# Performance work log

Measured on AMD Instinct MI355X. Metric: run time of the kernel, lower is better.

Reference implementation:

```python
import math
import jax, jax.numpy as jnp
import numpy as np

B, S, D, H = 4, 2048, 1024, 16
HD = D // H  # head_dim = 64


def setup_inputs() -> dict:
    key = jax.random.key(0)
    ks = jax.random.split(key, 10)
    scale = 1.0 / math.sqrt(D)
    inp = {
        "q": jax.random.normal(ks[0], (B, S, D), dtype=jnp.float32),
        "q_mask": jax.random.bernoulli(ks[1], 0.9, (B, S)),
        "Wq": jax.random.normal(ks[2], (D, D), dtype=jnp.float32) * scale,
        "bq": jax.random.normal(ks[3], (D,), dtype=jnp.float32) * 0.01,
        "Wk": jax.random.normal(ks[4], (D, D), dtype=jnp.float32) * scale,
        "bk": jax.random.normal(ks[5], (D,), dtype=jnp.float32) * 0.01,
        "Wv": jax.random.normal(ks[6], (D, D), dtype=jnp.float32) * scale,
        "bv": jax.random.normal(ks[7], (D,), dtype=jnp.float32) * 0.01,
        "Wo": jax.random.normal(ks[8], (D, D), dtype=jnp.float32) * scale,
        "bo": jax.random.normal(ks[9], (D,), dtype=jnp.float32) * 0.01,
    }
    return inp


def reference(q, q_mask, Wq, bq, Wk, bk, Wv, bv, Wo, bo):
    # Self-attention: k = v = q, kv_mask = q_mask (per forward() defaults).
    # Linear projections (nn.Linear: x @ W^T + b), then split heads -> (b, h, s, hd)
    def proj(x, W, b):
        y = jnp.einsum("bsd,ed->bse", x, W) + b
        return y.reshape(B, S, H, HD).transpose(0, 2, 1, 3)

    qh = proj(q, Wq, bq)
    kh = proj(q, Wk, bk)
    vh = proj(q, Wv, bv)

    # Scaled dot-product scores: (b, h, s_q, s_k), scaled by sqrt(head_dim)
    scores = jnp.einsum("bhqd,bhkd->bhqk", qh, kh) / math.sqrt(HD)

    # merge_masks: q_mask & kv_mask (kv_mask == q_mask), broadcast over heads
    merged = q_mask[:, :, None] & q_mask[:, None, :]          # (b, s_q, s_k)
    scores = jnp.where(merged[:, None, :, :], scores, -jnp.inf)

    # softmax over keys; fully-masked (padded query) rows -> nan -> 0
    attn = jax.nn.softmax(scores, axis=-1)
    attn = jnp.nan_to_num(attn, nan=0.0)
    # dropout prob = 0 (eval) -> no-op

    out = jnp.einsum("bhqk,bhkd->bhqd", attn, vh)             # (b, h, s, hd)
    out = out.transpose(0, 2, 1, 3).reshape(B, S, D)
    return jnp.einsum("bsd,ed->bse", out, Wo) + bo
```

## Files before the change

### kernel.cpp

```cpp
#include <hip/hip_runtime.h>
#include <hip/hip_bf16.h>
#include <stdint.h>

typedef __bf16 v8y __attribute__((ext_vector_type(8)));
typedef _Float16 v8h __attribute__((ext_vector_type(8)));
typedef float  v4f __attribute__((ext_vector_type(4)));
typedef float  v16f __attribute__((ext_vector_type(16)));
typedef __hip_bfloat16 bf;

#define AS1 __attribute__((address_space(1)))
#define AS3 __attribute__((address_space(3)))

__device__ __forceinline__ void gload16(const bf* g, bf* l) {
  __builtin_amdgcn_global_load_lds((const AS1 uint32_t*)g, (AS3 uint32_t*)l, 16, 0, 0);
}

static constexpr int Bb = 4, Sdim = 2048, Ddim = 1024, Hn = 16, HD = 64;
static constexpr int Kd = 1024, Nd = 1024;
static constexpr int WSZ = Ddim * Ddim;
static constexpr float NEG = -1e30f;

__device__ __forceinline__ void stc(bf* p, float v)    { *p = __float2bfloat16(v); }
__device__ __forceinline__ void stc(float* p, float v) { *p = v; }

__device__ __forceinline__ uint32_t pkbf(float lo, float hi_) {
  union { bf h[2]; uint32_t u; } t;
  t.h[0] = __float2bfloat16(lo);
  t.h[1] = __float2bfloat16(hi_);
  return t.u;
}

__global__ __launch_bounds__(256)
void cvt_f16(const float* __restrict__ src, uint16_t* __restrict__ dst, int n) {
  const int i = (blockIdx.x * 256 + threadIdx.x) * 8;
  if (i >= n) return;
  const float4 a = *reinterpret_cast<const float4*>(src + i);
  const float4 b = *reinterpret_cast<const float4*>(src + i + 4);
  const float x[8] = {a.x, a.y, a.z, a.w, b.x, b.y, b.z, b.w};
  union { uint16_t h[8]; uint4 u; } U;
#pragma unroll
  for (int j = 0; j < 8; ++j) U.h[j] = __builtin_bit_cast(uint16_t, (_Float16)x[j]);
  *reinterpret_cast<uint4*>(dst + i) = U.u;
}

__global__ __launch_bounds__(256)
void cvt_w(const float* __restrict__ Wq, const float* __restrict__ Wk,
           const float* __restrict__ Wv, const float* __restrict__ Wo,
           uint16_t* __restrict__ wb) {
  const int i = (blockIdx.x * 256 + threadIdx.x) * 8;
  const int z = blockIdx.y;
  const float* src = z == 0 ? Wq : (z == 1 ? Wk : (z == 2 ? Wv : Wo));
  uint16_t* dst = wb + (size_t)WSZ * z;
  const float4 a = *reinterpret_cast<const float4*>(src + i);
  const float4 b = *reinterpret_cast<const float4*>(src + i + 4);
  const float x[8] = {a.x, a.y, a.z, a.w, b.x, b.y, b.z, b.w};
  union { uint16_t h[8]; uint4 u; } U;
  if (z < 3) {
#pragma unroll
    for (int j = 0; j < 8; ++j) U.h[j] = __builtin_bit_cast(uint16_t, (_Float16)x[j]);
  } else {
#pragma unroll
    for (int j = 0; j < 8; ++j) U.h[j] = __builtin_bit_cast(uint16_t, __float2bfloat16(x[j]));
  }
  *reinterpret_cast<uint4*>(dst + i) = U.u;
}

__global__ __launch_bounds__(256)
void maskpack(const int* __restrict__ mask, uint64_t* __restrict__ mp) {
  const int gid = blockIdx.x * 256 + threadIdx.x;
  const uint64_t bal = __ballot(mask[gid] != 0);
  if ((threadIdx.x & 63) == 0) mp[gid >> 6] = bal;
}

template<bool F16, bool HEADLAYOUT, typename TC>
__global__ __launch_bounds__(256)
void gemm_bt(const bf* __restrict__ A,
             const bf* __restrict__ W0, const bf* __restrict__ W1, const bf* __restrict__ W2,
             const float* __restrict__ b0, const float* __restrict__ b1, const float* __restrict__ b2,
             TC* __restrict__ C0, TC* __restrict__ C1, TC* __restrict__ C2)
{
  const int z = blockIdx.z;
  const bf* Wh = z == 0 ? W0 : (z == 1 ? W1 : W2);
  const float* bias = z == 0 ? b0 : (z == 1 ? b1 : b2);
  TC* C = z == 0 ? C0 : (z == 1 ? C1 : C2);

  constexpr int PL = 128 * 32;
  __shared__ __align__(16) bf As[PL];
  __shared__ __align__(16) bf Bs[PL];

  const int tid = threadIdx.x;
  const int w = tid >> 6, l = tid & 63;
  const int m0 = blockIdx.x * 128, n0 = blockIdx.y * 128;
  const int wm = (w & 1) * 64, wn = (w >> 1) * 64;
  const int lr = l & 15, quad = l >> 4;
  const int srow = l >> 2, sk = (l & 3) * 8;

  v4f acc[4][4] = {};

  for (int kt = 0; kt < Kd; kt += 32) {
    __syncthreads();
#pragma unroll
    for (int c = 0; c < 2; ++c) {
      const int rb = (c * 4 + w) * 16;
      const int64_t goff = (int64_t)(rb + srow) * Kd + kt + sk;
      gload16(A + (int64_t)m0 * Kd + goff, As + rb * 32);
      gload16(Wh + (int64_t)n0 * Kd + goff, Bs + rb * 32);
    }
    __syncthreads();

    v8y afh[4], bfh[4];
#pragma unroll
    for (int i = 0; i < 4; ++i) {
      const int ro = (wm + i * 16 + lr) * 32 + quad * 8;
      const int co = (wn + i * 16 + lr) * 32 + quad * 8;
      afh[i] = *reinterpret_cast<const v8y*>(As + ro);
      bfh[i] = *reinterpret_cast<const v8y*>(Bs + co);
    }
#pragma unroll
    for (int i = 0; i < 4; ++i)
#pragma unroll
      for (int j = 0; j < 4; ++j) {
        if constexpr (F16) {
          acc[i][j] = __builtin_amdgcn_mfma_f32_16x16x32_f16(
              __builtin_bit_cast(v8h, afh[i]), __builtin_bit_cast(v8h, bfh[j]),
              acc[i][j], 0, 0, 0);
        } else {
          acc[i][j] = __builtin_amdgcn_mfma_f32_16x16x32_bf16(afh[i], bfh[j], acc[i][j], 0, 0, 0);
        }
      }
  }

#pragma unroll
  for (int j = 0; j < 4; ++j) {
    const int gn = n0 + wn + j * 16 + lr;
    const float bv = bias[gn];
#pragma unroll
    for (int i = 0; i < 4; ++i) {
#pragma unroll
      for (int r = 0; r < 4; ++r) {
        const int gm = m0 + wm + i * 16 + quad * 4 + r;
        float v = acc[i][j][r] + bv;
        if (HEADLAYOUT) {
          const int bidx = gm >> 11, s = gm & (Sdim - 1);
          const int h = gn >> 6, hd = gn & (HD - 1);
          if (z == 0) v *= 0.125f;
          const int64_t idx = (z == 2)
            ? ((int64_t)(bidx * Hn + h) * HD + hd) * Sdim + s
            : (((int64_t)(bidx * Hn + h) * Sdim + s) << 6) + hd;
          stc(&C[idx], v);
        } else {
          stc(&C[(int64_t)gm * Nd + gn], v);
        }
      }
    }
  }
}

__global__ __launch_bounds__(256)
void attn_kernel(const bf* __restrict__ qh, const bf* __restrict__ kh,
                 const bf* __restrict__ vt, const int* __restrict__ mask,
                 const uint64_t* __restrict__ mp, bf* __restrict__ outp)
{
  __shared__ __align__(16) bf sm[2][8192];

  const int tid = threadIdx.x;
  const int w = tid >> 6, l = tid & 63;
  const int lq = l & 31, hi = l >> 5;
  const int bh = blockIdx.x, b = bh >> 4;
  const int q0 = blockIdx.y * 128 + w * 32;
  const int64_t base = (int64_t)bh * (Sdim * HD);

  v8y qf[4];
#pragma unroll
  for (int s = 0; s < 4; ++s)
    qf[s] = *reinterpret_cast<const v8y*>(qh + base + (int64_t)(q0 + lq) * 64 + s * 16 + hi * 8);

  const bool qmask = mask[b * Sdim + q0 + lq] != 0;

  float m_i = NEG, l_i = 0.f;
  v16f oacc[2] = {};

  const int srcperm = ((l & 7) ^ (l >> 3)) * 8;
  const int srow8 = l >> 3;

#define STAGE(bufi, ktn)                                                          \
  {                                                                               \
    bf* KB_ = sm[bufi];                                                           \
    bf* VB_ = sm[bufi] + 4096;                                                    \
    _Pragma("unroll")                                                             \
    for (int i_ = 0; i_ < 2; ++i_) {                                              \
      const int c_ = w * 2 + i_;                                                  \
      const int row_ = c_ * 8 + srow8;                                            \
      gload16(kh + base + (int64_t)((ktn) + row_) * 64 + srcperm, KB_ + c_ * 512);\
      gload16(vt + base + (int64_t)row_ * Sdim + (ktn) + srcperm, VB_ + c_ * 512);\
    }                                                                             \
  }

  STAGE(0, 0);
  asm volatile("s_waitcnt vmcnt(0)" ::: "memory");
  __syncthreads();

  for (int kt = 0; kt < Sdim; kt += 64) {
    const int buf = (kt >> 6) & 1;
    if (kt + 64 < Sdim) STAGE(buf ^ 1, kt + 64);

    const bf* KB = sm[buf];
    const bf* VB = sm[buf] + 4096;

    v16f sacc[2] = {};
    __builtin_amdgcn_s_setprio(1);
#pragma unroll
    for (int n = 0; n < 2; ++n) {
      const int row = n * 32 + lq;
      const int swz = (row & 7);
#pragma unroll
      for (int s = 0; s < 4; ++s) {
        const int colE = ((2 * s + hi) ^ swz) * 8;
        v8y kf = *reinterpret_cast<const v8y*>(KB + row * 64 + colE);
        sacc[n] = __builtin_amdgcn_mfma_f32_32x32x16_bf16(kf, qf[s], sacc[n], 0, 0, 0);
      }
    }
    __builtin_amdgcn_s_setprio(0);

    const uint64_t km64 = mp[b * 32 + (kt >> 6)];
    const uint32_t km0 = (uint32_t)km64 >> (4 * hi);
    const uint32_t km1 = (uint32_t)(km64 >> 32) >> (4 * hi);
#pragma unroll
    for (int r = 0; r < 16; ++r) {
      const uint32_t bit = 1u << ((r & 3) + 8 * (r >> 2));
      sacc[0][r] = (km0 & bit) ? sacc[0][r] : NEG;
      sacc[1][r] = (km1 & bit) ? sacc[1][r] : NEG;
    }

    float mx = NEG;
#pragma unroll
    for (int n = 0; n < 2; ++n)
#pragma unroll
      for (int r = 0; r < 16; ++r) mx = fmaxf(mx, sacc[n][r]);
    mx = fmaxf(mx, __shfl_xor(mx, 32));
    const float mn = fmaxf(m_i, mx);
    const float alpha = __expf(m_i - mn);
    m_i = mn;

    float sum = 0.f;
#pragma unroll
    for (int n = 0; n < 2; ++n)
#pragma unroll
      for (int r = 0; r < 16; ++r) {
        const float p = __expf(sacc[n][r] - mn);
        sacc[n][r] = p;
        sum += p;
      }
    sum += __shfl_xor(sum, 32);
    l_i = l_i * alpha + sum;
#pragma unroll
    for (int d2 = 0; d2 < 2; ++d2)
#pragma unroll
      for (int r = 0; r < 16; ++r) oacc[d2][r] *= alpha;

    uint32_t pq[8][2];
#pragma unroll
    for (int n = 0; n < 2; ++n)
#pragma unroll
      for (int g = 0; g < 4; ++g) {
        pq[n * 4 + g][0] = pkbf(sacc[n][g * 4 + 0], sacc[n][g * 4 + 1]);
        pq[n * 4 + g][1] = pkbf(sacc[n][g * 4 + 2], sacc[n][g * 4 + 3]);
      }

#pragma unroll
    for (int ks = 0; ks < 4; ++ks) {
      const uint32_t own0 = hi ? pq[2 * ks + 1][0] : pq[2 * ks][0];
      const uint32_t own1 = hi ? pq[2 * ks + 1][1] : pq[2 * ks][1];
      const uint32_t snd0 = hi ? pq[2 * ks][0] : pq[2 * ks + 1][0];
      const uint32_t snd1 = hi ? pq[2 * ks][1] : pq[2 * ks + 1][1];
      const uint32_t rc0 = (uint32_t)__shfl_xor((int)snd0, 32);
      const uint32_t rc1 = (uint32_t)__shfl_xor((int)snd1, 32);
      union { uint32_t u[4]; v8y v; } pf;
      pf.u[0] = hi ? rc0 : own0;
      pf.u[1] = hi ? rc1 : own1;
      pf.u[2] = hi ? own0 : rc0;
      pf.u[3] = hi ? own1 : rc1;
      __builtin_amdgcn_s_setprio(1);
#pragma unroll
      for (int d2 = 0; d2 < 2; ++d2) {
        const int row = d2 * 32 + lq;
        const int colE = ((2 * ks + hi) ^ (row & 7)) * 8;
        v8y vf = *reinterpret_cast<const v8y*>(VB + row * 64 + colE);
        oacc[d2] = __builtin_amdgcn_mfma_f32_32x32x16_bf16(vf, pf.v, oacc[d2], 0, 0, 0);
      }
      __builtin_amdgcn_s_setprio(0);
    }

    asm volatile("s_waitcnt vmcnt(0)" ::: "memory");
    __syncthreads();
  }
#undef STAGE

  const float inv = qmask ? 1.f / l_i : 0.f;
  bf* orow = outp + ((int64_t)b * Sdim + q0 + lq) * Ddim + (bh & 15) * 64;
#pragma unroll
  for (int d2 = 0; d2 < 2; ++d2)
#pragma unroll
    for (int g = 0; g < 4; ++g) {
      union { bf h[4]; uint2 u; } pk;
#pragma unroll
      for (int c = 0; c < 4; ++c) pk.h[c] = __float2bfloat16(oacc[d2][g * 4 + c] * inv);
      *reinterpret_cast<uint2*>(orow + d2 * 32 + 8 * g + 4 * hi) = pk.u;
    }
}

extern "C" void kernel_launch(void* const* d_in, const int* in_sizes, int n_in,
                              void* d_out, int out_size, void* d_ws, size_t ws_size,
                              hipStream_t stream) {
  (void)in_sizes; (void)n_in; (void)out_size; (void)ws_size;
  const float* q    = (const float*)d_in[0];
  const int*   mask = (const int*)d_in[1];
  const float* Wq = (const float*)d_in[2];
  const float* bq = (const float*)d_in[3];
  const float* Wk = (const float*)d_in[4];
  const float* bk = (const float*)d_in[5];
  const float* Wv = (const float*)d_in[6];
  const float* bv = (const float*)d_in[7];
  const float* Wo = (const float*)d_in[8];
  const float* bo = (const float*)d_in[9];
  float* out = (float*)d_out;
  bf* ws  = (bf*)d_ws;

  constexpr int SZ = Bb * Sdim * Ddim;

  bf* qc  = ws;
  bf* qhp = ws + (size_t)SZ;
  bf* khp = ws + 2 * (size_t)SZ;
  bf* vtp = ws + 3 * (size_t)SZ;
  bf* wb  = ws + 4 * (size_t)SZ;
  bf* wq = wb;
  bf* wk = wb + WSZ;
  bf* wv = wb + 2 * (size_t)WSZ;
  bf* wo = wb + 3 * (size_t)WSZ;
  uint64_t* mpk = (uint64_t*)(wb + 4 * (size_t)WSZ);
  bf* ao = qc;

  cvt_f16<<<dim3(SZ / 2048), dim3(256), 0, stream>>>(q, (uint16_t*)qc, SZ);
  cvt_w<<<dim3(WSZ / 2048, 4), dim3(256), 0, stream>>>(Wq, Wk, Wv, Wo, (uint16_t*)wb);
  maskpack<<<dim3(32), dim3(256), 0, stream>>>(mask, mpk);

  gemm_bt<true, true, bf><<<dim3(64, 8, 3), dim3(256), 0, stream>>>(
      qc, wq, wk, wv, bq, bk, bv, qhp, khp, vtp);

  attn_kernel<<<dim3(Bb * Hn, Sdim / 128), dim3(256), 0, stream>>>(qhp, khp, vtp, mask, mpk, ao);

  gemm_bt<false, false, float><<<dim3(64, 8, 1), dim3(256), 0, stream>>>(
      ao, wo, wo, wo, bo, bo, bo, out, out, out);
}
```

Baseline: 354.8 us.

## Rework attention softmax: exp2 scaling, lazy rescale, MFMA row sums, bitmask-AND masking

Folds log2(e) into the Q scale so the softmax can use exp2 directly. Skips the rescale of the running max and accumulator unless the new max exceeds the old one by more than a threshold. Replaces the per-lane sum reduction with an extra MFMA against a ones vector, and applies the key mask by ANDing the packed bf16 probabilities with precomputed 32-bit mask words. This removes per-element select, sum and scaling ALU work from the inner loop. In exchange it adds one MFMA per k-step, and the lazy rescale lets unnormalised probabilities grow to about 2^11, which reduces bf16 headroom.

```diff
diff --git a/kernel.cpp b/kernel.cpp
--- a/kernel.cpp
+++ b/kernel.cpp
@@ -19,6 +19,7 @@
 static constexpr int Kd = 1024, Nd = 1024;
 static constexpr int WSZ = Ddim * Ddim;
 static constexpr float NEG = -1e30f;
+static constexpr float QSCALE = 0.18033688011112042f;
 
 __device__ __forceinline__ void stc(bf* p, float v)    { *p = __float2bfloat16(v); }
 __device__ __forceinline__ void stc(float* p, float v) { *p = v; }
@@ -66,10 +67,19 @@
 }
 
 __global__ __launch_bounds__(256)
-void maskpack(const int* __restrict__ mask, uint64_t* __restrict__ mp) {
+void maskpack(const int* __restrict__ mask, uint32_t* __restrict__ mw) {
   const int gid = blockIdx.x * 256 + threadIdx.x;
   const uint64_t bal = __ballot(mask[gid] != 0);
-  if ((threadIdx.x & 63) == 0) mp[gid >> 6] = bal;
+  const int l = threadIdx.x & 63;
+  if (l < 32) {
+    const int bt = gid >> 6;
+    const int h = l >> 4, n = (l >> 3) & 1, g = (l >> 1) & 3, wi = l & 1;
+    const int k0 = n * 32 + g * 8 + h * 4 + wi * 2;
+    uint32_t wv = 0;
+    if ((bal >> k0) & 1) wv |= 0x0000FFFFu;
+    if ((bal >> (k0 + 1)) & 1) wv |= 0xFFFF0000u;
+    mw[bt * 32 + l] = wv;
+  }
 }
 
 template<bool F16, bool HEADLAYOUT, typename TC>
@@ -143,7 +153,7 @@
         if (HEADLAYOUT) {
           const int bidx = gm >> 11, s = gm & (Sdim - 1);
           const int h = gn >> 6, hd = gn & (HD - 1);
-          if (z == 0) v *= 0.125f;
+          if (z == 0) v *= QSCALE;
           const int64_t idx = (z == 2)
             ? ((int64_t)(bidx * Hn + h) * HD + hd) * Sdim + s
             : (((int64_t)(bidx * Hn + h) * Sdim + s) << 6) + hd;
@@ -159,7 +169,7 @@
 __global__ __launch_bounds__(256)
 void attn_kernel(const bf* __restrict__ qh, const bf* __restrict__ kh,
                  const bf* __restrict__ vt, const int* __restrict__ mask,
-                 const uint64_t* __restrict__ mp, bf* __restrict__ outp)
+                 const uint32_t* __restrict__ mw, bf* __restrict__ outp)
 {
   __shared__ __align__(16) bf sm[2][8192];
 
@@ -177,8 +187,13 @@
 
   const bool qmask = mask[b * Sdim + q0 + lq] != 0;
 
-  float m_i = NEG, l_i = 0.f;
+  union { uint32_t u[4]; v8y v; } ONES;
+#pragma unroll
+  for (int j = 0; j < 4; ++j) ONES.u[j] = 0x3F803F80u;
+
+  float m_i = NEG;
   v16f oacc[2] = {};
+  v16f sumacc = {};
 
   const int srcperm = ((l & 7) ^ (l >> 3)) * 8;
   const int srow8 = l >> 3;
@@ -204,6 +219,14 @@
     const int buf = (kt >> 6) & 1;
     if (kt + 64 < Sdim) STAGE(buf ^ 1, kt + 64);
 
+    union { uint32_t u[16]; uint4 q[4]; } MW;
+    {
+      const uint4* mwp = reinterpret_cast<const uint4*>(
+          mw + ((size_t)(b * 32 + (kt >> 6)) * 32) + hi * 16);
+#pragma unroll
+      for (int j = 0; j < 4; ++j) MW.q[j] = mwp[j];
+    }
+
     const bf* KB = sm[buf];
     const bf* VB = sm[buf] + 4096;
 
@@ -222,49 +245,36 @@
     }
     __builtin_amdgcn_s_setprio(0);
 
-    const uint64_t km64 = mp[b * 32 + (kt >> 6)];
-    const uint32_t km0 = (uint32_t)km64 >> (4 * hi);
-    const uint32_t km1 = (uint32_t)(km64 >> 32) >> (4 * hi);
-#pragma unroll
-    for (int r = 0; r < 16; ++r) {
-      const uint32_t bit = 1u << ((r & 3) + 8 * (r >> 2));
-      sacc[0][r] = (km0 & bit) ? sacc[0][r] : NEG;
-      sacc[1][r] = (km1 & bit) ? sacc[1][r] : NEG;
-    }
-
     float mx = NEG;
 #pragma unroll
     for (int n = 0; n < 2; ++n)
 #pragma unroll
       for (int r = 0; r < 16; ++r) mx = fmaxf(mx, sacc[n][r]);
     mx = fmaxf(mx, __shfl_xor(mx, 32));
-    const float mn = fmaxf(m_i, mx);
-    const float alpha = __expf(m_i - mn);
-    m_i = mn;
-
-    float sum = 0.f;
+
+    if (!__all(mx - m_i <= 11.0f)) {
+      const float mn = fmaxf(m_i, mx);
+      const float alpha = exp2f(m_i - mn);
+      m_i = mn;
+      sumacc[0] *= alpha;
+#pragma unroll
+      for (int d2 = 0; d2 < 2; ++d2)
+#pragma unroll
+        for (int r = 0; r < 16; ++r) oacc[d2][r] *= alpha;
+    }
+
 #pragma unroll
     for (int n = 0; n < 2; ++n)
 #pragma unroll
-      for (int r = 0; r < 16; ++r) {
-        const float p = __expf(sacc[n][r] - mn);
-        sacc[n][r] = p;
-        sum += p;
-      }
-    sum += __shfl_xor(sum, 32);
-    l_i = l_i * alpha + sum;
-#pragma unroll
-    for (int d2 = 0; d2 < 2; ++d2)
-#pragma unroll
-      for (int r = 0; r < 16; ++r) oacc[d2][r] *= alpha;
+      for (int r = 0; r < 16; ++r) sacc[n][r] = exp2f(sacc[n][r] - m_i);
 
     uint32_t pq[8][2];
 #pragma unroll
     for (int n = 0; n < 2; ++n)
 #pragma unroll
       for (int g = 0; g < 4; ++g) {
-        pq[n * 4 + g][0] = pkbf(sacc[n][g * 4 + 0], sacc[n][g * 4 + 1]);
-        pq[n * 4 + g][1] = pkbf(sacc[n][g * 4 + 2], sacc[n][g * 4 + 3]);
+        pq[n * 4 + g][0] = pkbf(sacc[n][g * 4 + 0], sacc[n][g * 4 + 1]) & MW.u[n * 8 + g * 2 + 0];
+        pq[n * 4 + g][1] = pkbf(sacc[n][g * 4 + 2], sacc[n][g * 4 + 3]) & MW.u[n * 8 + g * 2 + 1];
       }
 
 #pragma unroll
@@ -288,6 +298,7 @@
         v8y vf = *reinterpret_cast<const v8y*>(VB + row * 64 + colE);
         oacc[d2] = __builtin_amdgcn_mfma_f32_32x32x16_bf16(vf, pf.v, oacc[d2], 0, 0, 0);
       }
+      sumacc = __builtin_amdgcn_mfma_f32_32x32x16_bf16(ONES.v, pf.v, sumacc, 0, 0, 0);
       __builtin_amdgcn_s_setprio(0);
     }
 
@@ -296,7 +307,7 @@
   }
 #undef STAGE
 
-  const float inv = qmask ? 1.f / l_i : 0.f;
+  const float inv = qmask ? 1.f / sumacc[0] : 0.f;
   bf* orow = outp + ((int64_t)b * Sdim + q0 + lq) * Ddim + (bh & 15) * 64;
 #pragma unroll
   for (int d2 = 0; d2 < 2; ++d2)
@@ -337,17 +348,17 @@
   bf* wk = wb + WSZ;
   bf* wv = wb + 2 * (size_t)WSZ;
   bf* wo = wb + 3 * (size_t)WSZ;
-  uint64_t* mpk = (uint64_t*)(wb + 4 * (size_t)WSZ);
+  uint32_t* mw = (uint32_t*)(wb + 4 * (size_t)WSZ);
   bf* ao = qc;
 
   cvt_f16<<<dim3(SZ / 2048), dim3(256), 0, stream>>>(q, (uint16_t*)qc, SZ);
   cvt_w<<<dim3(WSZ / 2048, 4), dim3(256), 0, stream>>>(Wq, Wk, Wv, Wo, (uint16_t*)wb);
-  maskpack<<<dim3(32), dim3(256), 0, stream>>>(mask, mpk);
+  maskpack<<<dim3(32), dim3(256), 0, stream>>>(mask, mw);
 
   gemm_bt<true, true, bf><<<dim3(64, 8, 3), dim3(256), 0, stream>>>(
       qc, wq, wk, wv, bq, bk, bv, qhp, khp, vtp);
 
-  attn_kernel<<<dim3(Bb * Hn, Sdim / 128), dim3(256), 0, stream>>>(qhp, khp, vtp, mask, mpk, ao);
+  attn_kernel<<<dim3(Bb * Hn, Sdim / 128), dim3(256), 0, stream>>>(qhp, khp, vtp, mask, mw, ao);
 
   gemm_bt<false, false, float><<<dim3(64, 8, 1), dim3(256), 0, stream>>>(
       ao, wo, wo, wo, bo, bo, bo, out, out, out);
```

New measurement: 361.8 us. About the same (+2.0%).

## Fold log2e into Q scale, inject mask via MFMA bias, lazy rescale

Applied to the files above, without the earlier changes.

Folds log2(e) into the Q projection scale so softmax can use exp2 directly. Replaces the per-element bitmask select with an additive bf16 key bias that is loaded into LDS and injected as the initial accumulator through an extra rank-1 MFMA. The online-softmax rescale of the output accumulator is skipped unless some row's max grows by more than a threshold. The aim is to cut VALU work in the softmax loop, at the cost of two extra MFMAs per tile and a conditional rescale whose safety depends on the threshold bounding exp2 overflow.

```diff
diff --git a/kernel.cpp b/kernel.cpp
--- a/kernel.cpp
+++ b/kernel.cpp
@@ -19,6 +19,7 @@
 static constexpr int Kd = 1024, Nd = 1024;
 static constexpr int WSZ = Ddim * Ddim;
 static constexpr float NEG = -1e30f;
+static constexpr float QSCALE = 0.18033688011112042f;
 
 __device__ __forceinline__ void stc(bf* p, float v)    { *p = __float2bfloat16(v); }
 __device__ __forceinline__ void stc(float* p, float v) { *p = v; }
@@ -66,10 +67,9 @@
 }
 
 __global__ __launch_bounds__(256)
-void maskpack(const int* __restrict__ mask, uint64_t* __restrict__ mp) {
+void maskpack(const int* __restrict__ mask, bf* __restrict__ mbias) {
   const int gid = blockIdx.x * 256 + threadIdx.x;
-  const uint64_t bal = __ballot(mask[gid] != 0);
-  if ((threadIdx.x & 63) == 0) mp[gid >> 6] = bal;
+  mbias[gid] = __float2bfloat16(mask[gid] ? 0.f : NEG);
 }
 
 template<bool F16, bool HEADLAYOUT, typename TC>
@@ -143,7 +143,7 @@
         if (HEADLAYOUT) {
           const int bidx = gm >> 11, s = gm & (Sdim - 1);
           const int h = gn >> 6, hd = gn & (HD - 1);
-          if (z == 0) v *= 0.125f;
+          if (z == 0) v *= QSCALE;
           const int64_t idx = (z == 2)
             ? ((int64_t)(bidx * Hn + h) * HD + hd) * Sdim + s
             : (((int64_t)(bidx * Hn + h) * Sdim + s) << 6) + hd;
@@ -159,9 +159,10 @@
 __global__ __launch_bounds__(256)
 void attn_kernel(const bf* __restrict__ qh, const bf* __restrict__ kh,
                  const bf* __restrict__ vt, const int* __restrict__ mask,
-                 const uint64_t* __restrict__ mp, bf* __restrict__ outp)
+                 const bf* __restrict__ mbias, bf* __restrict__ outp)
 {
   __shared__ __align__(16) bf sm[2][8192];
+  __shared__ __align__(16) bf mb_lds[2048];
 
   const int tid = threadIdx.x;
   const int w = tid >> 6, l = tid & 63;
@@ -170,12 +171,19 @@
   const int q0 = blockIdx.y * 128 + w * 32;
   const int64_t base = (int64_t)bh * (Sdim * HD);
 
+  *reinterpret_cast<uint4*>(mb_lds + tid * 8) =
+      *reinterpret_cast<const uint4*>(mbias + b * Sdim + tid * 8);
+
   v8y qf[4];
 #pragma unroll
   for (int s = 0; s < 4; ++s)
     qf[s] = *reinterpret_cast<const v8y*>(qh + base + (int64_t)(q0 + lq) * 64 + s * 16 + hi * 8);
 
   const bool qmask = mask[b * Sdim + q0 + lq] != 0;
+
+  union { uint32_t u[4]; v8y v; } MB1;
+  MB1.u[0] = hi ? 0u : 0x00003F80u;
+  MB1.u[1] = 0; MB1.u[2] = 0; MB1.u[3] = 0;
 
   float m_i = NEG, l_i = 0.f;
   v16f oacc[2] = {};
@@ -207,7 +215,16 @@
     const bf* KB = sm[buf];
     const bf* VB = sm[buf] + 4096;
 
-    v16f sacc[2] = {};
+    union { uint32_t u[4]; v8y v; } MA0, MA1;
+    MA0.u[0] = (uint32_t)*reinterpret_cast<const uint16_t*>(mb_lds + kt + lq);
+    MA0.u[1] = 0; MA0.u[2] = 0; MA0.u[3] = 0;
+    MA1.u[0] = (uint32_t)*reinterpret_cast<const uint16_t*>(mb_lds + kt + 32 + lq);
+    MA1.u[1] = 0; MA1.u[2] = 0; MA1.u[3] = 0;
+    const v16f zz = {};
+    v16f sacc[2];
+    sacc[0] = __builtin_amdgcn_mfma_f32_32x32x16_bf16(MA0.v, MB1.v, zz, 0, 0, 0);
+    sacc[1] = __builtin_amdgcn_mfma_f32_32x32x16_bf16(MA1.v, MB1.v, zz, 0, 0, 0);
+
     __builtin_amdgcn_s_setprio(1);
 #pragma unroll
     for (int n = 0; n < 2; ++n) {
@@ -222,41 +239,36 @@
     }
     __builtin_amdgcn_s_setprio(0);
 
-    const uint64_t km64 = mp[b * 32 + (kt >> 6)];
-    const uint32_t km0 = (uint32_t)km64 >> (4 * hi);
-    const uint32_t km1 = (uint32_t)(km64 >> 32) >> (4 * hi);
-#pragma unroll
-    for (int r = 0; r < 16; ++r) {
-      const uint32_t bit = 1u << ((r & 3) + 8 * (r >> 2));
-      sacc[0][r] = (km0 & bit) ? sacc[0][r] : NEG;
-      sacc[1][r] = (km1 & bit) ? sacc[1][r] : NEG;
-    }
-
     float mx = NEG;
 #pragma unroll
     for (int n = 0; n < 2; ++n)
 #pragma unroll
-      for (int r = 0; r < 16; ++r) mx = fmaxf(mx, sacc[n][r]);
+      for (int r = 0; r < 16; r += 2)
+        mx = fmaxf(mx, fmaxf(sacc[n][r], sacc[n][r + 1]));
     mx = fmaxf(mx, __shfl_xor(mx, 32));
-    const float mn = fmaxf(m_i, mx);
-    const float alpha = __expf(m_i - mn);
-    m_i = mn;
+
+    if (!__all(mx - m_i <= 11.0f)) {
+      const float mn = fmaxf(m_i, mx);
+      const float alpha = exp2f(m_i - mn);
+      m_i = mn;
+      l_i *= alpha;
+#pragma unroll
+      for (int d2 = 0; d2 < 2; ++d2)
+#pragma unroll
+        for (int r = 0; r < 16; ++r) oacc[d2][r] *= alpha;
+    }
 
     float sum = 0.f;
 #pragma unroll
     for (int n = 0; n < 2; ++n)
 #pragma unroll
       for (int r = 0; r < 16; ++r) {
-        const float p = __expf(sacc[n][r] - mn);
+        const float p = exp2f(sacc[n][r] - m_i);
         sacc[n][r] = p;
         sum += p;
       }
     sum += __shfl_xor(sum, 32);
-    l_i = l_i * alpha + sum;
-#pragma unroll
-    for (int d2 = 0; d2 < 2; ++d2)
-#pragma unroll
-      for (int r = 0; r < 16; ++r) oacc[d2][r] *= alpha;
+    l_i += sum;
 
     uint32_t pq[8][2];
 #pragma unroll
@@ -337,17 +349,17 @@
   bf* wk = wb + WSZ;
   bf* wv = wb + 2 * (size_t)WSZ;
   bf* wo = wb + 3 * (size_t)WSZ;
-  uint64_t* mpk = (uint64_t*)(wb + 4 * (size_t)WSZ);
+  bf* mbias = wb + 4 * (size_t)WSZ;
   bf* ao = qc;
 
   cvt_f16<<<dim3(SZ / 2048), dim3(256), 0, stream>>>(q, (uint16_t*)qc, SZ);
   cvt_w<<<dim3(WSZ / 2048, 4), dim3(256), 0, stream>>>(Wq, Wk, Wv, Wo, (uint16_t*)wb);
-  maskpack<<<dim3(32), dim3(256), 0, stream>>>(mask, mpk);
+  maskpack<<<dim3(32), dim3(256), 0, stream>>>(mask, mbias);
 
   gemm_bt<true, true, bf><<<dim3(64, 8, 3), dim3(256), 0, stream>>>(
       qc, wq, wk, wv, bq, bk, bv, qhp, khp, vtp);
 
-  attn_kernel<<<dim3(Bb * Hn, Sdim / 128), dim3(256), 0, stream>>>(qhp, khp, vtp, mask, mpk, ao);
+  attn_kernel<<<dim3(Bb * Hn, Sdim / 128), dim3(256), 0, stream>>>(qhp, khp, vtp, mask, mbias, ao);
 
   gemm_bt<false, false, float><<<dim3(64, 8, 1), dim3(256), 0, stream>>>(
       ao, wo, wo, wo, bo, bo, bo, out, out, out);
```

Result: slower. 368.5 us (+3.9%).
